# Kernel optimization log

Measured on AMD Instinct MI355X. Metric: run time of the kernel, lower is better.

The kernel has to match this reference:

```python
import jax, jax.numpy as jnp
import numpy as np

NUM_CODES = 1024
CODE_DIM = 256
COMMITMENT_COST = 0.25
B, T = 32, 1024


def setup_inputs() -> dict:
    key = jax.random.key(0)
    k1, k2 = jax.random.split(key)
    latents = jax.random.normal(k1, (B, CODE_DIM, T), dtype=jnp.float32)
    # faithful to nn.Embedding init uniform_(-1/num_codes, 1/num_codes)
    codebook = jax.random.uniform(k2, (NUM_CODES, CODE_DIM), dtype=jnp.float32,
                                  minval=-1.0 / NUM_CODES, maxval=1.0 / NUM_CODES)
    return {"latents": latents, "codebook": codebook}


def reference(latents, codebook):
    # latents: [B, D, T], codebook: [K, D]
    b, d, t = latents.shape
    flat = jnp.transpose(latents, (0, 2, 1)).reshape(-1, d)  # [B*T, D]
    distances = (jnp.sum(flat * flat, axis=1, keepdims=True)
                 - 2.0 * flat @ codebook.T
                 + jnp.sum(codebook * codebook, axis=1))  # [B*T, K]
    indices = jnp.argmin(distances, axis=1)  # [B*T]
    quantized = codebook[indices].reshape(b, t, d).transpose(0, 2, 1)  # [B, D, T]
    codebook_loss = jnp.mean((quantized - jax.lax.stop_gradient(latents)) ** 2)
    commitment_loss = jnp.mean((jax.lax.stop_gradient(quantized) - latents) ** 2)
    loss = codebook_loss + COMMITMENT_COST * commitment_loss
    # straight-through estimator
    quantized_st = latents + jax.lax.stop_gradient(quantized - latents)
    return quantized_st, loss, indices.reshape(b, t)
```

## Files before the change

### kernel.cpp

```cpp
#include <hip/hip_runtime.h>
#include <math.h>

#define Dd 256
#define Tt 1024
#define Bb 32
#define Kk 1024
#define NROWS (Bb*Tt)
#define OUTQ  (Bb*Dd*Tt)
#define SLACK 4e-4f
#define LIST_CAP 458752u
#define CANDB_CAP 1024u

typedef __bf16 b16x8 __attribute__((ext_vector_type(8)));
typedef float  f32x4 __attribute__((ext_vector_type(4)));

#define OFF_LOSS  0
#define OFF_GCNT  8
#define OFF_W2    256
#define OFF_X2    8192
#define OFF_IDX   139264
#define OFF_PACK  270336
#define OFF_GMIN  532480
#define OFF_RMING 663552
#define OFF_LIST  1712128
#define OFF_BT    5382144
#define OFF_X     5906432
#define OFF_A     39460864
#define MIN_WS    (OFF_A + (size_t)NROWS*Dd*2)

__device__ __forceinline__ void gload16(const void* g, void* l) {
    __builtin_amdgcn_global_load_lds(
        (const __attribute__((address_space(1))) void*)g,
        (__attribute__((address_space(3))) void*)l, 16, 0, 0);
}

__global__ void vq_w2(const float* __restrict__ cb, float* __restrict__ w2f) {
#pragma clang fp contract(off)
    const int k = blockIdx.x * 256 + threadIdx.x;
    if (k >= Kk) return;
    const float* w = cb + (size_t)k * Dd;
    float h[2];
    for (int half = 0; half < 2; ++half) {
        const float* p = w + half * 128;
        float r[8];
        for (int j = 0; j < 8; ++j) { float v = p[j]; r[j] = v * v; }
        for (int m = 1; m < 16; ++m)
            for (int j = 0; j < 8; ++j) { float v = p[m*8 + j]; r[j] += v * v; }
        h[half] = ((r[0]+r[1]) + (r[2]+r[3])) + ((r[4]+r[5]) + (r[6]+r[7]));
    }
    w2f[k] = h[0] + h[1];
}

__global__ __launch_bounds__(256) void vq_cbprep(const float* __restrict__ cb,
                                                 float* __restrict__ w2f,
                                                 __bf16* __restrict__ BT) {
    __shared__ float wrow[256];
    const int c = blockIdx.x, t = threadIdx.x;
    float v = cb[(size_t)c*Dd + t];
    wrow[t] = v;
    BT[(size_t)c*Dd + t] = (__bf16)v;
    __syncthreads();
    if (t < 64) {
        float s = 0.0f;
        if (t < 16) {
#pragma clang fp contract(off)
            const int h = t >> 3, j = t & 7;
            float u = wrow[h*128 + j];
            float r8 = u * u;
            for (int m = 1; m < 16; ++m) {
                u = wrow[h*128 + m*8 + j];
                r8 += u * u;
            }
            s = r8;
        }
        s += __shfl_xor(s, 1, 64);
        s += __shfl_xor(s, 2, 64);
        s += __shfl_xor(s, 4, 64);
        s += __shfl_xor(s, 8, 64);
        if (t == 0) w2f[c] = s;
    }
}

__global__ void vq_prep_a(const float* __restrict__ lat, float* __restrict__ X,
                          __bf16* __restrict__ A) {
    __shared__ float tl[64][65];
    const int tid = threadIdx.x;
    const int rowbase = blockIdx.x * 64;
    const int b = rowbase >> 10, t0 = rowbase & 1023;
    const int d0 = blockIdx.y * 64;
    const int tt = tid & 63, sub = tid >> 6;
#pragma unroll
    for (int it = 0; it < 16; ++it) {
        int d = it*4 + sub;
        tl[d][tt] = lat[((size_t)(b*Dd + d0 + d))*Tt + t0 + tt];
    }
    __syncthreads();
    const int dd = tid & 63;
#pragma unroll
    for (int it = 0; it < 16; ++it) {
        int t = it*4 + sub;
        float v = tl[dd][t];
        int grow = rowbase + t;
        X[(size_t)grow*Dd + d0 + dd] = v;
        A[(size_t)grow*Dd + d0 + dd] = (__bf16)v;
    }
}

__global__ __launch_bounds__(256) void vq_x2(const float* __restrict__ X,
                                             float* __restrict__ x2f) {
    __shared__ float xrow[4][256];
    const int tid = threadIdx.x;
    const int wv = tid >> 6, l = tid & 63;
    const int row = blockIdx.x * 4 + wv;

    const float4* xg = (const float4*)(X + (size_t)row * Dd);
    *(float4*)&xrow[wv][l*4] = xg[l];
    __syncthreads();

    float s = 0.0f;
    if (l < 16) {
#pragma clang fp contract(off)
        const int h = l >> 3, j = l & 7;
        float v = xrow[wv][h*128 + j];
        float r8 = v * v;
        for (int m = 1; m < 16; ++m) {
            v = xrow[wv][h*128 + m*8 + j];
            r8 += v * v;
        }
        s = r8;
    }
    s += __shfl_xor(s, 1, 64);
    s += __shfl_xor(s, 2, 64);
    s += __shfl_xor(s, 4, 64);
    s += __shfl_xor(s, 8, 64);
    if (l == 0) x2f[row] = s;
}

__global__ __launch_bounds__(256) void vq_gemm(const __bf16* __restrict__ A,
                                               const __bf16* __restrict__ BT,
                                               const float* __restrict__ w2f,
                                               unsigned* __restrict__ gcnt,
                                               uint2* __restrict__ list,
                                               float* __restrict__ rming) {
    __shared__ __align__(16) char smem[65536];
    float (*rminS)[2] = (float(*)[2])smem;
    unsigned* nCand   = (unsigned*)(smem + 1024);
    unsigned* baseS   = (unsigned*)(smem + 1032);
    unsigned* candRC  = (unsigned*)(smem + 2048);
    float*    candF   = (float*)(smem + 6144);

    const int tid = threadIdx.x;
    const unsigned orig = blockIdx.x;
    const unsigned wgid = (orig & 7) * 256 + (orig >> 3);
    const int bn = wgid & 7, bm = wgid >> 3;
    const int l = tid & 63, wv = tid >> 6;
    const int wm = (wv & 1) * 64, wn = (wv >> 1) * 64;
    const int m16 = l & 15, quad = l >> 4;

    f32x4 acc[4][4];
#pragma unroll
    for (int i = 0; i < 4; ++i)
#pragma unroll
        for (int j = 0; j < 4; ++j) acc[i][j] = (f32x4){0.f,0.f,0.f,0.f};

    const int r8  = l >> 3;
    const int c8  = l & 7;
    const int csw = ((c8 ^ r8) * 8);
    const int sw  = m16 & 7;
    const size_t abase = (size_t)(bm*128) * Dd;
    const size_t bbase = (size_t)(bn*128) * Dd;

    auto stage = [&](int kt, int bsel) {
        char* dstA = smem + bsel*32768;
        char* dstB = smem + bsel*32768 + 16384;
        const int k0 = kt * 64;
#pragma unroll
        for (int p = 0; p < 4; ++p) {
            const int R0 = wv*32 + p*8;
            gload16(&A [abase + (size_t)(R0 + r8)*Dd + k0 + csw], dstA + R0*128);
            gload16(&BT[bbase + (size_t)(R0 + r8)*Dd + k0 + csw], dstB + R0*128);
        }
    };
    auto compute = [&](int bsel) {
        const char* As = smem + bsel*32768;
        const char* Bs = smem + bsel*32768 + 16384;
#pragma unroll
        for (int ks = 0; ks < 64; ks += 32) {
            const int k8 = ks >> 3;
            b16x8 a[4], b[4];
#pragma unroll
            for (int i = 0; i < 4; ++i)
                a[i] = *(const b16x8*)(As + (wm + 16*i + m16)*128 + (((k8 + quad) ^ sw) * 16));
#pragma unroll
            for (int j = 0; j < 4; ++j)
                b[j] = *(const b16x8*)(Bs + (wn + 16*j + m16)*128 + (((k8 + quad) ^ sw) * 16));
#pragma unroll
            for (int i = 0; i < 4; ++i)
#pragma unroll
                for (int j = 0; j < 4; ++j)
                    acc[i][j] = __builtin_amdgcn_mfma_f32_16x16x32_bf16(a[i], b[j], acc[i][j], 0, 0, 0);
        }
    };

    stage(0, 0);
    __syncthreads();
#pragma unroll
    for (int kt = 0; kt < 3; ++kt) {
        stage(kt + 1, (kt + 1) & 1);
        compute(kt & 1);
        __syncthreads();
    }
    compute(1);

    float w2n[4];
#pragma unroll
    for (int j = 0; j < 4; ++j) w2n[j] = w2f[bn*128 + wn + 16*j + m16];

    float vmin[4][4];
#pragma unroll
    for (int i = 0; i < 4; ++i)
#pragma unroll
        for (int g = 0; g < 4; ++g) {
            float v = w2n[0] - 2.0f * acc[i][0][g];
#pragma unroll
            for (int j = 1; j < 4; ++j)
                v = fminf(v, w2n[j] - 2.0f * acc[i][j][g]);
#pragma unroll
            for (int off = 1; off <= 8; off <<= 1)
                v = fminf(v, __shfl_xor(v, off, 64));
            vmin[i][g] = v;
        }
    if (m16 == 0) {
#pragma unroll
        for (int i = 0; i < 4; ++i)
#pragma unroll
            for (int g = 0; g < 4; ++g)
                rminS[wm + 16*i + quad*4 + g][wn >> 6] = vmin[i][g];
    }
    if (tid == 0) *nCand = 0u;
    __syncthreads();
    if (tid < 128)
        rming[((size_t)(bm*128 + tid))*8 + bn] = fminf(rminS[tid][0], rminS[tid][1]);
#pragma unroll
    for (int i = 0; i < 4; ++i)
#pragma unroll
        for (int g = 0; g < 4; ++g) {
            const int rloc = wm + 16*i + quad*4 + g;
            const float thr = fminf(rminS[rloc][0], rminS[rloc][1]) + SLACK;
#pragma unroll
            for (int j = 0; j < 4; ++j) {
                float f = w2n[j] - 2.0f * acc[i][j][g];
                if (f <= thr) {
                    unsigned slot = atomicAdd(nCand, 1u);
                    if (slot < CANDB_CAP) {
                        candRC[slot] = ((unsigned)(bm*128 + rloc) << 10)
                                     | (unsigned)(bn*128 + wn + 16*j + m16);
                        candF[slot]  = f;
                    }
                }
            }
        }
    __syncthreads();
    unsigned nc = *nCand; if (nc > CANDB_CAP) nc = CANDB_CAP;
    if (tid == 0) *baseS = atomicAdd(gcnt, nc);
    __syncthreads();
    const unsigned base = *baseS;
    for (unsigned i = tid; i < nc; i += 256) {
        unsigned dst = base + i;
        if (dst < LIST_CAP) {
            uint2 e; e.x = candRC[i]; e.y = __float_as_uint(candF[i]);
            list[dst] = e;
        }
    }
}

__global__ __launch_bounds__(256) void vq_gmin(const float* __restrict__ rming,
                                               float* __restrict__ gmin) {
    const int row = blockIdx.x * 256 + threadIdx.x;
    const float4* p = (const float4*)(rming + (size_t)row * 8);
    float4 a = p[0], b = p[1];
    float m = fminf(fminf(fminf(a.x, a.y), fminf(a.z, a.w)),
                    fminf(fminf(b.x, b.y), fminf(b.z, b.w)));
    gmin[row] = m + SLACK;
}

__global__ __launch_bounds__(256) void vq_rescore(const float* __restrict__ X,
                                                  const float* __restrict__ cb,
                                                  const float* __restrict__ w2f,
                                                  const float* __restrict__ x2f,
                                                  const float* __restrict__ gmin,
                                                  const unsigned* __restrict__ gcnt,
                                                  const uint2* __restrict__ list,
                                                  unsigned long long* __restrict__ pack) {
    unsigned n = *gcnt; if (n > LIST_CAP) n = LIST_CAP;
    const unsigned stride = gridDim.x * 256u;
    for (unsigned i = blockIdx.x * 256u + threadIdx.x; i < n; i += stride) {
        const uint2 e = list[i];
        const int row = (int)(e.x >> 10);
        const int c   = (int)(e.x & 1023u);
        if (__uint_as_float(e.y) > gmin[row]) continue;

        const float4* wq = (const float4*)(cb + (size_t)c * Dd);
        const float4* xq = (const float4*)(X + (size_t)row * Dd);
        float acc = 0.0f;
#pragma unroll 8
        for (int m = 0; m < 64; ++m) {
            float4 xa = xq[m], wa = wq[m];
            acc = __builtin_fmaf(xa.x, wa.x, acc);
            acc = __builtin_fmaf(xa.y, wa.y, acc);
            acc = __builtin_fmaf(xa.z, wa.z, acc);
            acc = __builtin_fmaf(xa.w, wa.w, acc);
        }
        float t2 = x2f[row] - 2.0f * acc;
        float dv = t2 + w2f[c];
        unsigned long long pk = ((unsigned long long)__float_as_uint(dv) << 32)
                              | (unsigned long long)(unsigned)c;
        atomicMin(&pack[row], pk);
    }
}

__global__ __launch_bounds__(256) void vq_pick(const unsigned long long* __restrict__ pack,
                                               int* __restrict__ idx,
                                               float* __restrict__ out,
                                               double* __restrict__ loss_acc) {
    __shared__ double wsum[4];
    const int tid = threadIdx.x;
    const int row = blockIdx.x * 256 + tid;
    const unsigned long long pk = pack[row];
    const int cc = (int)(pk & 0xFFFFFFFFull);
    idx[row] = cc;
    out[OUTQ + 1 + row] = (float)cc;
    double d = (double)__uint_as_float((unsigned)(pk >> 32));
    for (int off = 32; off; off >>= 1) d += __shfl_xor(d, off, 64);
    if ((tid & 63) == 0) wsum[tid >> 6] = d;
    __syncthreads();
    if (tid == 0) atomicAdd(loss_acc, wsum[0] + wsum[1] + wsum[2] + wsum[3]);
}

typedef float float8_t __attribute__((ext_vector_type(8)));
__global__ __launch_bounds__(512) void vq_main(const float* __restrict__ latents,
                                               const float* __restrict__ cb,
                                               const float* __restrict__ w2f,
                                               int* __restrict__ idx,
                                               double* __restrict__ loss_acc) {
    __shared__ float  xs[Dd*64];
    __shared__ float  x2f[64];
    __shared__ float  bsd[8*64];
    __shared__ int    bci[8*64];
    __shared__ double red[64];
    const int tid = threadIdx.x;
    const int rr  = tid & 63;
    const int dg  = tid >> 6;
    const int blk = blockIdx.x;
    const int bb  = blk >> 4;
    const int t0  = (blk & 15) << 6;
    const float* lat = latents + (size_t)bb * Dd * Tt + t0;
    for (int d = dg; d < Dd; d += 8) xs[d*64 + rr] = lat[(size_t)d * Tt + rr];
    __syncthreads();
    if (tid < 64) {
#pragma clang fp contract(off)
        float h[2];
        for (int half = 0; half < 2; ++half) {
            float r[8];
            for (int j = 0; j < 8; ++j) { float v = xs[(half*128 + j)*64 + tid]; r[j] = v*v; }
            for (int m = 1; m < 16; ++m)
                for (int j = 0; j < 8; ++j) { float v = xs[(half*128 + m*8 + j)*64 + tid]; r[j] += v*v; }
            h[half] = ((r[0]+r[1]) + (r[2]+r[3])) + ((r[4]+r[5]) + (r[6]+r[7]));
        }
        x2f[tid] = h[0] + h[1];
    }
    __syncthreads();
    const int slab = __builtin_amdgcn_readfirstlane(tid >> 6);
    const int lane = tid & 63;
    const float x2r = x2f[lane];
    const float* wq = cb + (size_t)slab * 128 * Dd;
    float best = 3.4e38f; int bestc = 0;
    for (int cg = 0; cg < 16; ++cg) {
        const int c0 = cg * 8;
        float acc[8];
#pragma unroll
        for (int g = 0; g < 8; ++g) acc[g] = 0.0f;
        for (int kc = 0; kc < 32; ++kc) {
            float8_t w8[8];
#pragma unroll
            for (int g = 0; g < 8; ++g) w8[g] = *(const float8_t*)(wq + (size_t)(c0+g)*Dd + kc*8);
            float xk[8];
#pragma unroll
            for (int j = 0; j < 8; ++j) xk[j] = xs[(kc*8 + j)*64 + lane];
#pragma unroll
            for (int g = 0; g < 8; ++g)
#pragma unroll
                for (int j = 0; j < 8; ++j) acc[g] = __builtin_fmaf(xk[j], w8[g][j], acc[g]);
        }
#pragma unroll
        for (int g = 0; g < 8; ++g) {
            float t2 = x2r - 2.0f * acc[g];
            float dvv = t2 + w2f[slab*128 + c0 + g];
            if (dvv < best) { best = dvv; bestc = slab*128 + c0 + g; }
        }
    }
    bsd[slab*64 + lane] = best; bci[slab*64 + lane] = bestc;
    __syncthreads();
    if (tid < 64) {
        float b0 = bsd[tid]; int ci = bci[tid];
#pragma unroll
        for (int s = 1; s < 8; ++s) { float b1 = bsd[s*64 + tid]; if (b1 < b0) { b0 = b1; ci = bci[s*64 + tid]; } }
        idx[blk*64 + tid] = ci; red[tid] = (double)b0;
    }
    __syncthreads();
    if (tid == 0) { double s = 0.0; for (int i = 0; i < 64; ++i) s += red[i]; atomicAdd(loss_acc, s); }
}

__global__ void vq_gather(const float* __restrict__ cb,
                          const int* __restrict__ idx,
                          float* __restrict__ out) {
    const size_t g = (size_t)blockIdx.x * 256 + threadIdx.x;
    const int t  = (int)(g & 1023);
    const int d4 = (int)((g >> 10) & 63);
    const int b  = (int)(g >> 16);
    const int i  = idx[b*Tt + t];
    const float4 w4 = *(const float4*)(cb + (size_t)i*Dd + d4*4);
    float* o = out + ((size_t)(b*Dd + d4*4)) * Tt + t;
    o[0]    = w4.x;
    o[Tt]   = w4.y;
    o[2*Tt] = w4.z;
    o[3*Tt] = w4.w;
}

__global__ void vq_finalize(const double* __restrict__ loss_acc,
                            float* __restrict__ out) {
    out[OUTQ] = (float)(1.25 * loss_acc[0] / (double)OUTQ);
}

__global__ void vq_idxf(const int* __restrict__ idx, float* __restrict__ out) {
    const int r = blockIdx.x * 256 + threadIdx.x;
    if (r < NROWS) out[OUTQ + 1 + r] = (float)idx[r];
}

extern "C" void kernel_launch(void* const* d_in, const int* in_sizes, int n_in,
                              void* d_out, int out_size, void* d_ws, size_t ws_size,
                              hipStream_t stream) {
    const float* latents = (const float*)d_in[0];
    const float* cb      = (const float*)d_in[1];
    float* out = (float*)d_out;
    char*  ws  = (char*)d_ws;

    double* loss = (double*)(ws + OFF_LOSS);
    float*  w2f  = (float*)(ws + OFF_W2);
    int*    idx  = (int*)(ws + OFF_IDX);

    hipMemsetAsync(ws, 0, 16, stream);

    if (ws_size >= (size_t)MIN_WS) {
        unsigned*           gcnt  = (unsigned*)(ws + OFF_GCNT);
        float*              x2f   = (float*)(ws + OFF_X2);
        unsigned long long* pack  = (unsigned long long*)(ws + OFF_PACK);
        float*              gmin  = (float*)(ws + OFF_GMIN);
        float*              rming = (float*)(ws + OFF_RMING);
        uint2*              list  = (uint2*)(ws + OFF_LIST);
        __bf16*             BT    = (__bf16*)(ws + OFF_BT);
        float*              X     = (float*)(ws + OFF_X);
        __bf16*             A     = (__bf16*)(ws + OFF_A);

        hipMemsetAsync(pack, 0xFF, sizeof(unsigned long long) * NROWS, stream);
        vq_cbprep<<<Kk, 256, 0, stream>>>(cb, w2f, BT);
        vq_prep_a<<<dim3(NROWS/64, 4), 256, 0, stream>>>(latents, X, A);
        vq_x2<<<NROWS/4, 256, 0, stream>>>(X, x2f);
        vq_gemm<<<2048, 256, 0, stream>>>(A, BT, w2f, gcnt, list, rming);
        vq_gmin<<<NROWS/256, 256, 0, stream>>>(rming, gmin);
        vq_rescore<<<1024, 256, 0, stream>>>(X, cb, w2f, x2f, gmin, gcnt, list, pack);
        vq_pick<<<NROWS/256, 256, 0, stream>>>(pack, idx, out, loss);
    } else {
        vq_w2<<<4, 256, 0, stream>>>(cb, w2f);
        vq_main<<<NROWS/64, 512, 0, stream>>>(latents, cb, w2f, idx, loss);
        vq_idxf<<<(NROWS + 255)/256, 256, 0, stream>>>(idx, out);
    }

    vq_gather<<<(Bb*(Dd/4)*Tt)/256, 256, 0, stream>>>(cb, idx, out);
    vq_finalize<<<1, 1, 0, stream>>>(loss, out);
}
```

Before: 198.3 us.

## Fuse row-norm into transpose prep and replace gmin pass with atomic min

Computes the per-row squared norm inside the transpose/prep kernel from shared memory, which removes the separate vq_x2 kernel and its re-read of X. The GEMM now writes each tile's row minimum straight into a per-row global minimum via atomicMin on a monotonic float-to-uint encoding, which removes the rming buffer and the vq_gmin kernel. The pack memset is enlarged so one fill also initialises gminU to the max encoding. This saves two launches and some traffic, at the cost of atomic contention and a prep kernel with fewer blocks and more shared memory per block.

After: 216.1 us. 9.0% more time.

```diff
diff --git a/kernel.cpp b/kernel.cpp
--- a/kernel.cpp
+++ b/kernel.cpp
@@ -20,18 +20,26 @@
 #define OFF_X2    8192
 #define OFF_IDX   139264
 #define OFF_PACK  270336
-#define OFF_GMIN  532480
-#define OFF_RMING 663552
-#define OFF_LIST  1712128
-#define OFF_BT    5382144
-#define OFF_X     5906432
-#define OFF_A     39460864
+#define OFF_GMINU 532480
+#define OFF_LIST  663552
+#define OFF_BT    4333568
+#define OFF_X     4857856
+#define OFF_A     38412288
 #define MIN_WS    (OFF_A + (size_t)NROWS*Dd*2)
 
 __device__ __forceinline__ void gload16(const void* g, void* l) {
     __builtin_amdgcn_global_load_lds(
         (const __attribute__((address_space(1))) void*)g,
         (__attribute__((address_space(3))) void*)l, 16, 0, 0);
+}
+
+__device__ __forceinline__ unsigned fmono(float f) {
+    unsigned b = __float_as_uint(f);
+    return b ^ ((unsigned)((int)b >> 31) | 0x80000000u);
+}
+__device__ __forceinline__ float fmono_inv(unsigned u) {
+    unsigned b = (u & 0x80000000u) ? (u ^ 0x80000000u) : ~u;
+    return __uint_as_float(b);
 }
 
 __global__ void vq_w2(const float* __restrict__ cb, float* __restrict__ w2f) {
@@ -81,59 +89,61 @@
     }
 }
 
-__global__ void vq_prep_a(const float* __restrict__ lat, float* __restrict__ X,
-                          __bf16* __restrict__ A) {
-    __shared__ float tl[64][65];
+__global__ __launch_bounds__(256) void vq_prep_a(const float* __restrict__ lat,
+                                                 float* __restrict__ X,
+                                                 __bf16* __restrict__ A,
+                                                 float* __restrict__ x2f) {
+    __shared__ float tl[128][65];
     const int tid = threadIdx.x;
     const int rowbase = blockIdx.x * 64;
     const int b = rowbase >> 10, t0 = rowbase & 1023;
-    const int d0 = blockIdx.y * 64;
     const int tt = tid & 63, sub = tid >> 6;
-#pragma unroll
-    for (int it = 0; it < 16; ++it) {
-        int d = it*4 + sub;
-        tl[d][tt] = lat[((size_t)(b*Dd + d0 + d))*Tt + t0 + tt];
-    }
-    __syncthreads();
-    const int dd = tid & 63;
-#pragma unroll
-    for (int it = 0; it < 16; ++it) {
-        int t = it*4 + sub;
-        float v = tl[dd][t];
-        int grow = rowbase + t;
-        X[(size_t)grow*Dd + d0 + dd] = v;
-        A[(size_t)grow*Dd + d0 + dd] = (__bf16)v;
-    }
-}
-
-__global__ __launch_bounds__(256) void vq_x2(const float* __restrict__ X,
-                                             float* __restrict__ x2f) {
-    __shared__ float xrow[4][256];
-    const int tid = threadIdx.x;
     const int wv = tid >> 6, l = tid & 63;
-    const int row = blockIdx.x * 4 + wv;
-
-    const float4* xg = (const float4*)(X + (size_t)row * Dd);
-    *(float4*)&xrow[wv][l*4] = xg[l];
-    __syncthreads();
-
-    float s = 0.0f;
-    if (l < 16) {
+    const int g = l >> 4, l4 = l & 15, hh = l4 >> 3, jj = l4 & 7;
+    const int dloc = tid & 127, trow2 = tid >> 7;
+
+    float r8p[4];
+
+    for (int half = 0; half < 2; ++half) {
+#pragma unroll
+        for (int it = 0; it < 32; ++it) {
+            int d = it*4 + sub;
+            tl[d][tt] = lat[((size_t)(b*Dd + half*128 + d))*Tt + t0 + tt];
+        }
+        __syncthreads();
+#pragma unroll
+        for (int it = 0; it < 32; ++it) {
+            int t = it*2 + trow2;
+            float v = tl[dloc][t];
+            size_t off = (size_t)(rowbase + t)*Dd + half*128 + dloc;
+            X[off] = v;
+            A[off] = (__bf16)v;
+        }
+#pragma unroll
+        for (int pass = 0; pass < 4; ++pass) {
+            int t = pass*16 + wv*4 + g;
+            if (hh == half) {
 #pragma clang fp contract(off)
-        const int h = l >> 3, j = l & 7;
-        float v = xrow[wv][h*128 + j];
-        float r8 = v * v;
-        for (int m = 1; m < 16; ++m) {
-            v = xrow[wv][h*128 + m*8 + j];
-            r8 += v * v;
-        }
-        s = r8;
-    }
-    s += __shfl_xor(s, 1, 64);
-    s += __shfl_xor(s, 2, 64);
-    s += __shfl_xor(s, 4, 64);
-    s += __shfl_xor(s, 8, 64);
-    if (l == 0) x2f[row] = s;
+                float v = tl[jj][t];
+                float r8 = v * v;
+                for (int m = 1; m < 16; ++m) {
+                    v = tl[m*8 + jj][t];
+                    r8 += v * v;
+                }
+                r8p[pass] = r8;
+            }
+        }
+        __syncthreads();
+    }
+#pragma unroll
+    for (int pass = 0; pass < 4; ++pass) {
+        float s = r8p[pass];
+        s += __shfl_xor(s, 1, 64);
+        s += __shfl_xor(s, 2, 64);
+        s += __shfl_xor(s, 4, 64);
+        s += __shfl_xor(s, 8, 64);
+        if (l4 == 0) x2f[rowbase + pass*16 + wv*4 + g] = s;
+    }
 }
 
 __global__ __launch_bounds__(256) void vq_gemm(const __bf16* __restrict__ A,
@@ -141,7 +151,7 @@
                                                const float* __restrict__ w2f,
                                                unsigned* __restrict__ gcnt,
                                                uint2* __restrict__ list,
-                                               float* __restrict__ rming) {
+                                               unsigned* __restrict__ gminU) {
     __shared__ __align__(16) char smem[65536];
     float (*rminS)[2] = (float(*)[2])smem;
     unsigned* nCand   = (unsigned*)(smem + 1024);
@@ -240,7 +250,7 @@
     if (tid == 0) *nCand = 0u;
     __syncthreads();
     if (tid < 128)
-        rming[((size_t)(bm*128 + tid))*8 + bn] = fminf(rminS[tid][0], rminS[tid][1]);
+        atomicMin(&gminU[bm*128 + tid], fmono(fminf(rminS[tid][0], rminS[tid][1])));
 #pragma unroll
     for (int i = 0; i < 4; ++i)
 #pragma unroll
@@ -274,21 +284,11 @@
     }
 }
 
-__global__ __launch_bounds__(256) void vq_gmin(const float* __restrict__ rming,
-                                               float* __restrict__ gmin) {
-    const int row = blockIdx.x * 256 + threadIdx.x;
-    const float4* p = (const float4*)(rming + (size_t)row * 8);
-    float4 a = p[0], b = p[1];
-    float m = fminf(fminf(fminf(a.x, a.y), fminf(a.z, a.w)),
-                    fminf(fminf(b.x, b.y), fminf(b.z, b.w)));
-    gmin[row] = m + SLACK;
-}
-
 __global__ __launch_bounds__(256) void vq_rescore(const float* __restrict__ X,
                                                   const float* __restrict__ cb,
                                                   const float* __restrict__ w2f,
                                                   const float* __restrict__ x2f,
-                                                  const float* __restrict__ gmin,
+                                                  const unsigned* __restrict__ gminU,
                                                   const unsigned* __restrict__ gcnt,
                                                   const uint2* __restrict__ list,
                                                   unsigned long long* __restrict__ pack) {
@@ -298,7 +298,8 @@
         const uint2 e = list[i];
         const int row = (int)(e.x >> 10);
         const int c   = (int)(e.x & 1023u);
-        if (__uint_as_float(e.y) > gmin[row]) continue;
+        const float gm = fmono_inv(gminU[row]);
+        if (__uint_as_float(e.y) > gm + SLACK) continue;
 
         const float4* wq = (const float4*)(cb + (size_t)c * Dd);
         const float4* xq = (const float4*)(X + (size_t)row * Dd);
@@ -455,20 +456,17 @@
         unsigned*           gcnt  = (unsigned*)(ws + OFF_GCNT);
         float*              x2f   = (float*)(ws + OFF_X2);
         unsigned long long* pack  = (unsigned long long*)(ws + OFF_PACK);
-        float*              gmin  = (float*)(ws + OFF_GMIN);
-        float*              rming = (float*)(ws + OFF_RMING);
+        unsigned*           gminU = (unsigned*)(ws + OFF_GMINU);
         uint2*              list  = (uint2*)(ws + OFF_LIST);
         __bf16*             BT    = (__bf16*)(ws + OFF_BT);
         float*              X     = (float*)(ws + OFF_X);
         __bf16*             A     = (__bf16*)(ws + OFF_A);
 
-        hipMemsetAsync(pack, 0xFF, sizeof(unsigned long long) * NROWS, stream);
+        hipMemsetAsync(pack, 0xFF, 393216, stream);
         vq_cbprep<<<Kk, 256, 0, stream>>>(cb, w2f, BT);
-        vq_prep_a<<<dim3(NROWS/64, 4), 256, 0, stream>>>(latents, X, A);
-        vq_x2<<<NROWS/4, 256, 0, stream>>>(X, x2f);
-        vq_gemm<<<2048, 256, 0, stream>>>(A, BT, w2f, gcnt, list, rming);
-        vq_gmin<<<NROWS/256, 256, 0, stream>>>(rming, gmin);
-        vq_rescore<<<1024, 256, 0, stream>>>(X, cb, w2f, x2f, gmin, gcnt, list, pack);
+        vq_prep_a<<<NROWS/64, 256, 0, stream>>>(latents, X, A, x2f);
+        vq_gemm<<<2048, 256, 0, stream>>>(A, BT, w2f, gcnt, list, gminU);
+        vq_rescore<<<1024, 256, 0, stream>>>(X, cb, w2f, x2f, gminU, gcnt, list, pack);
         vq_pick<<<NROWS/256, 256, 0, stream>>>(pack, idx, out, loss);
     } else {
         vq_w2<<<4, 256, 0, stream>>>(cb, w2f);
```
